# Performance work log

Measured on AMD Instinct MI355X. Metric: run time of the kernel, lower is better.

## Reference

```python
import jax, jax.numpy as jnp
import numpy as np

N_ATOM_TYPES = 100
N_BOND_TYPES = 10
N_NODES = 10000
N_EDGES = 320000
N_CAND = 100000
HID = 256
N_MP = 3


def setup_inputs() -> dict:
    key = jax.random.key(0)
    ks = jax.random.split(key, 16)
    d = HID
    inp = {
        "atom_types": jax.random.randint(ks[0], (N_NODES,), 0, N_ATOM_TYPES),
        "bond_types": jax.random.randint(ks[1], (N_EDGES,), 0, N_BOND_TYPES),
        "edge_index": jax.random.randint(ks[2], (2, N_EDGES), 0, N_NODES),
        "candidates": jax.random.randint(ks[3], (N_CAND, 2), 0, N_NODES),
        # parameters (weights stored as [in, out]; bias [out])
        "atom_embed": jax.random.normal(ks[4], (N_ATOM_TYPES, d)) * 0.02,
        "atom_W": jax.random.normal(ks[5], (d, d)) / np.sqrt(d),
        "atom_b": jnp.zeros((d,)),
        "bond_embed": jax.random.normal(ks[6], (N_BOND_TYPES, d)) * 0.02,
        "bond_W": jax.random.normal(ks[7], (d, d)) / np.sqrt(d),
        "bond_b": jnp.zeros((d,)),
        "conv_W": jax.random.normal(ks[8], (N_MP, d, d)) / np.sqrt(d),
        "conv_b": jnp.zeros((N_MP, d)),
        "s_W1": jax.random.normal(ks[9], (2 * d, d)) / np.sqrt(2 * d),
        "s_b1": jnp.zeros((d,)),
        "s_W2": jax.random.normal(ks[10], (d, 1)) / np.sqrt(d),
        "s_b2": jnp.zeros((1,)),
    }
    return inp


def _wln_forward(atom_types, bond_types, edge_index, candidates,
                 atom_embed, atom_W, atom_b, bond_embed, bond_W, bond_b,
                 conv_W, conv_b, s_W1, s_b1, s_W2, s_b2):
    # encoders
    h = atom_embed[atom_types] @ atom_W + atom_b            # [N, d]
    e = bond_embed[bond_types] @ bond_W + bond_b            # [E, d] (unused downstream, as in the original forward)
    del e

    src, dst = edge_index[0], edge_index[1]
    n = h.shape[0]
    ones = jnp.ones((src.shape[0],), dtype=h.dtype)
    deg_out = jax.ops.segment_sum(ones, src, num_segments=n)
    deg_in = jax.ops.segment_sum(ones, dst, num_segments=n)
    norm_src = jnp.where(deg_out > 0, deg_out ** -0.5, 0.0)[:, None]  # [N,1]
    norm_dst = jnp.where(deg_in > 0, deg_in ** -0.5, 0.0)[:, None]

    # message passing: DGL GraphConv norm='both' + ReLU
    for i in range(conv_W.shape[0]):
        m = (h * norm_src)[src]                             # [E, d]
        agg = jax.ops.segment_sum(m, dst, num_segments=n)   # [N, d]
        h = jax.nn.relu((agg * norm_dst) @ conv_W[i] + conv_b[i])

    # batched candidate scorer: gather + concat + 2-layer MLP
    u, v = candidates[:, 0], candidates[:, 1]
    pair = jnp.concatenate([h[u], h[v]], axis=-1)           # [C, 2d]
    hid = jax.nn.relu(pair @ s_W1 + s_b1)                   # [C, d]
    scores = hid @ s_W2 + s_b2                              # [C, 1]
    return scores.squeeze(-1)                               # [C]


def reference(atom_types, bond_types, edge_index, candidates,
              atom_embed, atom_W, atom_b, bond_embed, bond_W, bond_b,
              conv_W, conv_b, s_W1, s_b1, s_W2, s_b2):
    return _wln_forward(atom_types, bond_types, edge_index, candidates,
                        atom_embed, atom_W, atom_b, bond_embed, bond_W, bond_b,
                        conv_W, conv_b, s_W1, s_b1, s_W2, s_b2)
```

## Files before the change

### kernel.cpp

```cpp
#include <hip/hip_runtime.h>

#define N_NODES 10000
#define N_EDGES 320000
#define N_CAND  100000
#define HID     256
#define N_MP    3
#define N_ATYPE 100

static __device__ __forceinline__ float relu_f(float x) { return x > 0.f ? x : 0.f; }

__global__ __launch_bounds__(256) void k_gemm(
    const float* __restrict__ A, const float* __restrict__ B,
    const float* __restrict__ bias, float* __restrict__ C,
    int M, int doRelu)
{
    const int K = 256;
    __shared__ float As[32][68];
    __shared__ float Bs[32][64];

    int tid = threadIdx.x;
    int tx = tid & 15;
    int ty = tid >> 4;
    int mb = blockIdx.x * 64;
    int nb = blockIdx.y * 64;

    int ar = tid >> 3;
    int ac = tid & 7;
    int bc = tid & 15;
    int brw = tid >> 4;

    float acc[4][4] = {};

    for (int k0 = 0; k0 < K; k0 += 32) {
        #pragma unroll
        for (int h = 0; h < 2; ++h) {
            int row = mb + ar + h * 32;
            float4 av = make_float4(0.f, 0.f, 0.f, 0.f);
            if (row < M) av = *(const float4*)(A + (long)row * K + k0 + ac * 4);
            As[ac * 4 + 0][ar + h * 32] = av.x;
            As[ac * 4 + 1][ar + h * 32] = av.y;
            As[ac * 4 + 2][ar + h * 32] = av.z;
            As[ac * 4 + 3][ar + h * 32] = av.w;
        }
        #pragma unroll
        for (int h = 0; h < 2; ++h) {
            int k = brw + h * 16;
            *(float4*)(&Bs[k][bc * 4]) =
                *(const float4*)(B + (long)(k0 + k) * 256 + nb + bc * 4);
        }
        __syncthreads();

        #pragma unroll
        for (int k = 0; k < 32; ++k) {
            float4 a4 = *(const float4*)(&As[k][ty * 4]);
            float4 b4 = *(const float4*)(&Bs[k][tx * 4]);
            float a[4] = {a4.x, a4.y, a4.z, a4.w};
            float b[4] = {b4.x, b4.y, b4.z, b4.w};
            #pragma unroll
            for (int i = 0; i < 4; ++i)
                #pragma unroll
                for (int j = 0; j < 4; ++j)
                    acc[i][j] = fmaf(a[i], b[j], acc[i][j]);
        }
        __syncthreads();
    }

    float bvv[4] = {0.f, 0.f, 0.f, 0.f};
    if (bias) {
        float4 bv = *(const float4*)(bias + nb + tx * 4);
        bvv[0] = bv.x; bvv[1] = bv.y; bvv[2] = bv.z; bvv[3] = bv.w;
    }
    #pragma unroll
    for (int i = 0; i < 4; ++i) {
        int row = mb + ty * 4 + i;
        if (row >= M) break;
        float r[4];
        #pragma unroll
        for (int j = 0; j < 4; ++j) {
            r[j] = acc[i][j] + bvv[j];
            if (doRelu) r[j] = relu_f(r[j]);
        }
        float4 st = make_float4(r[0], r[1], r[2], r[3]);
        *(float4*)(C + (long)row * 256 + nb + tx * 4) = st;
    }
}

__global__ void k_hist(const int* __restrict__ ei,
                       int* __restrict__ dout, int* __restrict__ din)
{
    int e = blockIdx.x * blockDim.x + threadIdx.x;
    if (e >= N_EDGES) return;
    atomicAdd(&dout[ei[e]], 1);
    atomicAdd(&din[ei[N_EDGES + e]], 1);
}

__global__ void k_norm(const int* __restrict__ dout, const int* __restrict__ din,
                       float* __restrict__ ns, float* __restrict__ nd)
{
    int i = blockIdx.x * blockDim.x + threadIdx.x;
    if (i >= N_NODES) return;
    int o = dout[i], in = din[i];
    ns[i] = (o  > 0) ? (1.0f / sqrtf((float)o))  : 0.f;
    nd[i] = (in > 0) ? (1.0f / sqrtf((float)in)) : 0.f;
}

__global__ __launch_bounds__(256) void k_h0(const int* __restrict__ types,
                                            const float* __restrict__ E0,
                                            float* __restrict__ h)
{
    int node = blockIdx.x * 4 + (threadIdx.x >> 6);
    int lane = threadIdx.x & 63;
    if (node >= N_NODES) return;
    int t = types[node];
    ((float4*)h)[node * 64 + lane] = ((const float4*)E0)[t * 64 + lane];
}

__global__ __launch_bounds__(256) void k_scan(const int* __restrict__ deg,
                                              int* __restrict__ off, int n)
{
    __shared__ int part[256];
    int t = threadIdx.x;
    int chunk = (n + 255) / 256;
    int base = t * chunk;
    int s = 0;
    for (int i = 0; i < chunk; ++i) {
        int idx = base + i;
        if (idx < n) s += deg[idx];
    }
    part[t] = s;
    __syncthreads();
    for (int d = 1; d < 256; d <<= 1) {
        int v = (t >= d) ? part[t - d] : 0;
        __syncthreads();
        part[t] += v;
        __syncthreads();
    }
    int run = (t == 0) ? 0 : part[t - 1];
    if (t == 0) off[0] = 0;
    for (int i = 0; i < chunk; ++i) {
        int idx = base + i;
        if (idx < n) { run += deg[idx]; off[idx + 1] = run; }
    }
}

__global__ void k_fill(const int* __restrict__ ei, const int* __restrict__ off,
                       int* __restrict__ cur, int* __restrict__ csr)
{
    int e = blockIdx.x * blockDim.x + threadIdx.x;
    if (e >= N_EDGES) return;
    int d = ei[N_EDGES + e];
    int p = off[d] + atomicAdd(&cur[d], 1);
    csr[p] = ei[e];
}

__global__ __launch_bounds__(256) void k_agg(
    const float* __restrict__ h, const float* __restrict__ ns,
    const float* __restrict__ nd, const int* __restrict__ off,
    const int* __restrict__ csr, float* __restrict__ out)
{
    int node = blockIdx.x * 4 + (threadIdx.x >> 6);
    int lane = threadIdx.x & 63;
    if (node >= N_NODES) return;
    int s0 = off[node], s1 = off[node + 1];
    float4 acc = make_float4(0.f, 0.f, 0.f, 0.f);
    for (int e = s0; e < s1; ++e) {
        int s = csr[e];
        float w = ns[s];
        float4 hv = ((const float4*)h)[s * 64 + lane];
        acc.x = fmaf(hv.x, w, acc.x);
        acc.y = fmaf(hv.y, w, acc.y);
        acc.z = fmaf(hv.z, w, acc.z);
        acc.w = fmaf(hv.w, w, acc.w);
    }
    float d = nd[node];
    acc.x *= d; acc.y *= d; acc.z *= d; acc.w *= d;
    ((float4*)out)[node * 64 + lane] = acc;
}

__global__ __launch_bounds__(256) void k_score(
    const int* __restrict__ cand, const float* __restrict__ P,
    const float* __restrict__ Q, const float* __restrict__ b1,
    const float* __restrict__ W2, const float* __restrict__ b2,
    float* __restrict__ out)
{
    int c = blockIdx.x * 4 + (threadIdx.x >> 6);
    int lane = threadIdx.x & 63;
    if (c >= N_CAND) return;
    int u = cand[2 * c];
    int v = cand[2 * c + 1];
    float4 p = ((const float4*)P)[u * 64 + lane];
    float4 q = ((const float4*)Q)[v * 64 + lane];
    float4 b = ((const float4*)b1)[lane];
    float4 w = ((const float4*)W2)[lane];
    float hx = relu_f(p.x + q.x + b.x);
    float hy = relu_f(p.y + q.y + b.y);
    float hz = relu_f(p.z + q.z + b.z);
    float hw = relu_f(p.w + q.w + b.w);
    float d = hx * w.x + hy * w.y + hz * w.z + hw * w.w;
    #pragma unroll
    for (int o = 32; o > 0; o >>= 1)
        d += __shfl_xor(d, o, 64);
    if (lane == 0) out[c] = d + b2[0];
}

extern "C" void kernel_launch(void* const* d_in, const int* in_sizes, int n_in,
                              void* d_out, int out_size, void* d_ws, size_t ws_size,
                              hipStream_t stream)
{
    const int*   atom_types = (const int*)d_in[0];
    const int*   edge_index = (const int*)d_in[2];
    const int*   candidates = (const int*)d_in[3];
    const float* atom_embed = (const float*)d_in[4];
    const float* atom_W     = (const float*)d_in[5];
    const float* atom_b     = (const float*)d_in[6];
    const float* conv_W     = (const float*)d_in[10];
    const float* conv_b     = (const float*)d_in[11];
    const float* s_W1       = (const float*)d_in[12];
    const float* s_b1       = (const float*)d_in[13];
    const float* s_W2       = (const float*)d_in[14];
    const float* s_b2       = (const float*)d_in[15];
    float* out = (float*)d_out;

    char* w = (char*)d_ws;
    size_t o = 0;
    auto alloc = [&](size_t bytes) {
        void* p = w + o;
        o += (bytes + 255) & ~(size_t)255;
        return p;
    };
    float* h0  = (float*)alloc((size_t)N_NODES * HID * 4);
    float* h1  = (float*)alloc((size_t)N_NODES * HID * 4);
    float* agg = (float*)alloc((size_t)N_NODES * HID * 4);
    float* E0  = (float*)alloc((size_t)N_ATYPE * HID * 4);
    int*   ints = (int*)alloc((size_t)3 * N_NODES * 4);
    float* ns  = (float*)alloc((size_t)N_NODES * 4);
    float* nd  = (float*)alloc((size_t)N_NODES * 4);
    int*   off = (int*)alloc((size_t)(N_NODES + 1) * 4);
    int*   csr = (int*)alloc((size_t)N_EDGES * 4);
    int* dego = ints;
    int* degi = ints + N_NODES;
    int* cur  = ints + 2 * N_NODES;

    hipMemsetAsync(ints, 0, (size_t)3 * N_NODES * 4, stream);

    k_gemm<<<dim3(2, 4), 256, 0, stream>>>(atom_embed, atom_W, atom_b, E0, N_ATYPE, 0);

    k_hist<<<(N_EDGES + 255) / 256, 256, 0, stream>>>(edge_index, dego, degi);
    k_norm<<<(N_NODES + 255) / 256, 256, 0, stream>>>(dego, degi, ns, nd);
    k_h0<<<N_NODES / 4, 256, 0, stream>>>(atom_types, E0, h0);
    k_scan<<<1, 256, 0, stream>>>(degi, off, N_NODES);
    k_fill<<<(N_EDGES + 255) / 256, 256, 0, stream>>>(edge_index, off, cur, csr);

    const float* hc = h0;
    float* hn = h1;
    for (int i = 0; i < N_MP; ++i) {
        k_agg<<<N_NODES / 4, 256, 0, stream>>>(hc, ns, nd, off, csr, agg);
        k_gemm<<<dim3((N_NODES + 63) / 64, 4), 256, 0, stream>>>(
            agg, conv_W + (size_t)i * HID * HID, conv_b + (size_t)i * HID, hn, N_NODES, 1);
        float* t = (float*)hc; hc = hn; hn = t;
    }
    float* P = agg;
    float* Q = hn;
    k_gemm<<<dim3((N_NODES + 63) / 64, 4), 256, 0, stream>>>(hc, s_W1, nullptr, P, N_NODES, 0);
    k_gemm<<<dim3((N_NODES + 63) / 64, 4), 256, 0, stream>>>(hc, s_W1 + HID * HID, nullptr, Q, N_NODES, 0);

    k_score<<<N_CAND / 4, 256, 0, stream>>>(candidates, P, Q, s_b1, s_W2, s_b2, out);
}
```

Measured before the change: 405.5 us.

## Use 128-thread 8x4 GEMM microtile, merge P/Q GEMMs, unroll aggregation loop

The GEMM drops to 128 threads per 64x64 tile, with each thread computing an 8x4 block of outputs. This raises the arithmetic done per shared-memory load, and the B tile gets padding. The two scorer GEMMs (P and Q) now run as one launch over an 8-wide grid y-dimension. The CSR aggregation loop is unrolled by 4 with two accumulators, so more independent gather loads are in flight. The cost is more registers per thread and fewer threads per block, which may lower occupancy or latency hiding.

```diff
diff --git a/kernel.cpp b/kernel.cpp
--- a/kernel.cpp
+++ b/kernel.cpp
@@ -9,55 +9,53 @@
 
 static __device__ __forceinline__ float relu_f(float x) { return x > 0.f ? x : 0.f; }
 
-__global__ __launch_bounds__(256) void k_gemm(
+static __device__ __forceinline__ void gemm_core(
     const float* __restrict__ A, const float* __restrict__ B,
     const float* __restrict__ bias, float* __restrict__ C,
-    int M, int doRelu)
-{
-    const int K = 256;
+    int M, int mb, int nb, int doRelu)
+{
     __shared__ float As[32][68];
-    __shared__ float Bs[32][64];
+    __shared__ float Bs[32][68];
 
     int tid = threadIdx.x;
     int tx = tid & 15;
     int ty = tid >> 4;
-    int mb = blockIdx.x * 64;
-    int nb = blockIdx.y * 64;
-
-    int ar = tid >> 3;
-    int ac = tid & 7;
-    int bc = tid & 15;
-    int brw = tid >> 4;
-
-    float acc[4][4] = {};
-
-    for (int k0 = 0; k0 < K; k0 += 32) {
+
+    float acc[8][4] = {};
+
+    for (int k0 = 0; k0 < 256; k0 += 32) {
         #pragma unroll
-        for (int h = 0; h < 2; ++h) {
-            int row = mb + ar + h * 32;
+        for (int p = 0; p < 4; ++p) {
+            int flat = p * 128 + tid;
+            int row  = flat >> 3;
+            int kc   = flat & 7;
             float4 av = make_float4(0.f, 0.f, 0.f, 0.f);
-            if (row < M) av = *(const float4*)(A + (long)row * K + k0 + ac * 4);
-            As[ac * 4 + 0][ar + h * 32] = av.x;
-            As[ac * 4 + 1][ar + h * 32] = av.y;
-            As[ac * 4 + 2][ar + h * 32] = av.z;
-            As[ac * 4 + 3][ar + h * 32] = av.w;
+            if (mb + row < M)
+                av = *(const float4*)(A + (size_t)(mb + row) * 256 + k0 + kc * 4);
+            As[kc * 4 + 0][row] = av.x;
+            As[kc * 4 + 1][row] = av.y;
+            As[kc * 4 + 2][row] = av.z;
+            As[kc * 4 + 3][row] = av.w;
         }
         #pragma unroll
-        for (int h = 0; h < 2; ++h) {
-            int k = brw + h * 16;
-            *(float4*)(&Bs[k][bc * 4]) =
-                *(const float4*)(B + (long)(k0 + k) * 256 + nb + bc * 4);
+        for (int p = 0; p < 4; ++p) {
+            int flat = p * 128 + tid;
+            int row  = flat >> 4;
+            int c    = flat & 15;
+            *(float4*)(&Bs[row][c * 4]) =
+                *(const float4*)(B + (size_t)(k0 + row) * 256 + nb + c * 4);
         }
         __syncthreads();
 
         #pragma unroll
         for (int k = 0; k < 32; ++k) {
-            float4 a4 = *(const float4*)(&As[k][ty * 4]);
+            float4 a0 = *(const float4*)(&As[k][ty * 8]);
+            float4 a1 = *(const float4*)(&As[k][ty * 8 + 4]);
             float4 b4 = *(const float4*)(&Bs[k][tx * 4]);
-            float a[4] = {a4.x, a4.y, a4.z, a4.w};
+            float a[8] = {a0.x, a0.y, a0.z, a0.w, a1.x, a1.y, a1.z, a1.w};
             float b[4] = {b4.x, b4.y, b4.z, b4.w};
             #pragma unroll
-            for (int i = 0; i < 4; ++i)
+            for (int i = 0; i < 8; ++i)
                 #pragma unroll
                 for (int j = 0; j < 4; ++j)
                     acc[i][j] = fmaf(a[i], b[j], acc[i][j]);
@@ -71,18 +69,36 @@
         bvv[0] = bv.x; bvv[1] = bv.y; bvv[2] = bv.z; bvv[3] = bv.w;
     }
     #pragma unroll
-    for (int i = 0; i < 4; ++i) {
-        int row = mb + ty * 4 + i;
-        if (row >= M) break;
+    for (int i = 0; i < 8; ++i) {
+        int row = mb + ty * 8 + i;
+        if (row >= M) continue;
         float r[4];
         #pragma unroll
         for (int j = 0; j < 4; ++j) {
             r[j] = acc[i][j] + bvv[j];
             if (doRelu) r[j] = relu_f(r[j]);
         }
-        float4 st = make_float4(r[0], r[1], r[2], r[3]);
-        *(float4*)(C + (long)row * 256 + nb + tx * 4) = st;
-    }
+        *(float4*)(C + (size_t)row * 256 + nb + tx * 4) =
+            make_float4(r[0], r[1], r[2], r[3]);
+    }
+}
+
+__global__ __launch_bounds__(128) void k_gemm(
+    const float* __restrict__ A, const float* __restrict__ B,
+    const float* __restrict__ bias, float* __restrict__ C,
+    int M, int doRelu)
+{
+    gemm_core(A, B, bias, C, M, blockIdx.x * 64, blockIdx.y * 64, doRelu);
+}
+
+__global__ __launch_bounds__(128) void k_gemm_pq(
+    const float* __restrict__ A, const float* __restrict__ W1,
+    float* __restrict__ P, float* __restrict__ Q, int M)
+{
+    int half = blockIdx.y >> 2;
+    const float* B = W1 + (size_t)half * 256 * 256;
+    float* C = half ? Q : P;
+    gemm_core(A, B, nullptr, C, M, blockIdx.x * 64, (blockIdx.y & 3) * 64, 0);
 }
 
 __global__ void k_hist(const int* __restrict__ ei,
@@ -162,19 +178,42 @@
     int lane = threadIdx.x & 63;
     if (node >= N_NODES) return;
     int s0 = off[node], s1 = off[node + 1];
-    float4 acc = make_float4(0.f, 0.f, 0.f, 0.f);
-    for (int e = s0; e < s1; ++e) {
+    const float4* h4 = (const float4*)h;
+
+    float4 acc0 = make_float4(0.f, 0.f, 0.f, 0.f);
+    float4 acc1 = make_float4(0.f, 0.f, 0.f, 0.f);
+
+    int e = s0;
+    for (; e + 4 <= s1; e += 4) {
+        int i0 = csr[e], i1 = csr[e + 1], i2 = csr[e + 2], i3 = csr[e + 3];
+        float w0 = ns[i0], w1 = ns[i1], w2 = ns[i2], w3 = ns[i3];
+        float4 v0 = h4[(size_t)i0 * 64 + lane];
+        float4 v1 = h4[(size_t)i1 * 64 + lane];
+        float4 v2 = h4[(size_t)i2 * 64 + lane];
+        float4 v3 = h4[(size_t)i3 * 64 + lane];
+        acc0.x = fmaf(v0.x, w0, acc0.x); acc0.y = fmaf(v0.y, w0, acc0.y);
+        acc0.z = fmaf(v0.z, w0, acc0.z); acc0.w = fmaf(v0.w, w0, acc0.w);
+        acc1.x = fmaf(v1.x, w1, acc1.x); acc1.y = fmaf(v1.y, w1, acc1.y);
+        acc1.z = fmaf(v1.z, w1, acc1.z); acc1.w = fmaf(v1.w, w1, acc1.w);
+        acc0.x = fmaf(v2.x, w2, acc0.x); acc0.y = fmaf(v2.y, w2, acc0.y);
+        acc0.z = fmaf(v2.z, w2, acc0.z); acc0.w = fmaf(v2.w, w2, acc0.w);
+        acc1.x = fmaf(v3.x, w3, acc1.x); acc1.y = fmaf(v3.y, w3, acc1.y);
+        acc1.z = fmaf(v3.z, w3, acc1.z); acc1.w = fmaf(v3.w, w3, acc1.w);
+    }
+    for (; e < s1; ++e) {
         int s = csr[e];
         float w = ns[s];
-        float4 hv = ((const float4*)h)[s * 64 + lane];
-        acc.x = fmaf(hv.x, w, acc.x);
-        acc.y = fmaf(hv.y, w, acc.y);
-        acc.z = fmaf(hv.z, w, acc.z);
-        acc.w = fmaf(hv.w, w, acc.w);
+        float4 hv = h4[(size_t)s * 64 + lane];
+        acc0.x = fmaf(hv.x, w, acc0.x); acc0.y = fmaf(hv.y, w, acc0.y);
+        acc0.z = fmaf(hv.z, w, acc0.z); acc0.w = fmaf(hv.w, w, acc0.w);
     }
     float d = nd[node];
-    acc.x *= d; acc.y *= d; acc.z *= d; acc.w *= d;
-    ((float4*)out)[node * 64 + lane] = acc;
+    float4 r;
+    r.x = (acc0.x + acc1.x) * d;
+    r.y = (acc0.y + acc1.y) * d;
+    r.z = (acc0.z + acc1.z) * d;
+    r.w = (acc0.w + acc1.w) * d;
+    ((float4*)out)[node * 64 + lane] = r;
 }
 
 __global__ __launch_bounds__(256) void k_score(
@@ -188,8 +227,8 @@
     if (c >= N_CAND) return;
     int u = cand[2 * c];
     int v = cand[2 * c + 1];
-    float4 p = ((const float4*)P)[u * 64 + lane];
-    float4 q = ((const float4*)Q)[v * 64 + lane];
+    float4 p = ((const float4*)P)[(size_t)u * 64 + lane];
+    float4 q = ((const float4*)Q)[(size_t)v * 64 + lane];
     float4 b = ((const float4*)b1)[lane];
     float4 w = ((const float4*)W2)[lane];
     float hx = relu_f(p.x + q.x + b.x);
@@ -243,7 +282,7 @@
 
     hipMemsetAsync(ints, 0, (size_t)3 * N_NODES * 4, stream);
 
-    k_gemm<<<dim3(2, 4), 256, 0, stream>>>(atom_embed, atom_W, atom_b, E0, N_ATYPE, 0);
+    k_gemm<<<dim3(2, 4), 128, 0, stream>>>(atom_embed, atom_W, atom_b, E0, N_ATYPE, 0);
 
     k_hist<<<(N_EDGES + 255) / 256, 256, 0, stream>>>(edge_index, dego, degi);
     k_norm<<<(N_NODES + 255) / 256, 256, 0, stream>>>(dego, degi, ns, nd);
@@ -253,16 +292,16 @@
 
     const float* hc = h0;
     float* hn = h1;
+    const int GX = (N_NODES + 63) / 64;
     for (int i = 0; i < N_MP; ++i) {
         k_agg<<<N_NODES / 4, 256, 0, stream>>>(hc, ns, nd, off, csr, agg);
-        k_gemm<<<dim3((N_NODES + 63) / 64, 4), 256, 0, stream>>>(
+        k_gemm<<<dim3(GX, 4), 128, 0, stream>>>(
             agg, conv_W + (size_t)i * HID * HID, conv_b + (size_t)i * HID, hn, N_NODES, 1);
         float* t = (float*)hc; hc = hn; hn = t;
     }
     float* P = agg;
     float* Q = hn;
-    k_gemm<<<dim3((N_NODES + 63) / 64, 4), 256, 0, stream>>>(hc, s_W1, nullptr, P, N_NODES, 0);
-    k_gemm<<<dim3((N_NODES + 63) / 64, 4), 256, 0, stream>>>(hc, s_W1 + HID * HID, nullptr, Q, N_NODES, 0);
+    k_gemm_pq<<<dim3(GX, 8), 128, 0, stream>>>(hc, s_W1, P, Q, N_NODES);
 
     k_score<<<N_CAND / 4, 256, 0, stream>>>(candidates, P, Q, s_b1, s_W2, s_b2, out);
 }
```

Measured after the change: 418.2 us. 1.03x slower.
